# Kernel optimization log

Measured on AMD Instinct MI355X. Metric: run time of the kernel, lower is better.

Reference implementation:

```python
import jax, jax.numpy as jnp
import numpy as np
from jax import lax

B, HIST, FC, N, F = 64, 24, 24, 1000, 8
EMB, HID, NEMB, OUT = 32, 64, 1000, 1
IN = EMB + OUT  # GRU input dim


def setup_inputs() -> dict:
    key = jax.random.key(0)
    ks = jax.random.split(key, 11)
    X = jax.random.normal(ks[0], (B, HIST + FC, N, F), jnp.float32)
    idx = jax.random.randint(ks[1], (B, HIST + FC, N), 0, NEMB)
    X = X.at[..., -1].set(idx.astype(jnp.float32))  # last channel = spatial ids
    hn = jax.random.normal(ks[2], (B * N, HID), jnp.float32)
    xn = jax.random.normal(ks[3], (B, N, OUT), jnp.float32)
    s = 0.1
    emb_table = jax.random.normal(ks[4], (NEMB, EMB), jnp.float32) * s
    W_ih = jax.random.normal(ks[5], (3 * HID, IN), jnp.float32) * s
    W_hh = jax.random.normal(ks[6], (3 * HID, HID), jnp.float32) * s
    b_ih = jax.random.normal(ks[7], (3 * HID,), jnp.float32) * s
    b_hh = jax.random.normal(ks[8], (3 * HID,), jnp.float32) * s
    W_out = jax.random.normal(ks[9], (OUT, HID), jnp.float32) * s
    b_out = jax.random.normal(ks[10], (OUT,), jnp.float32) * s
    return {"X": X, "hn": hn, "xn": xn, "emb_table": emb_table,
            "W_ih": W_ih, "W_hh": W_hh, "b_ih": b_ih, "b_hh": b_hh,
            "W_out": W_out, "b_out": b_out}


def reference(X, hn, xn, emb_table, W_ih, W_hh, b_ih, b_hh, W_out, b_out):
    # indices for the forecast steps: [FC, B, N]
    idx_seq = X[:, :FC, :, -1].astype(jnp.int32).transpose(1, 0, 2)

    def step(carry, idx_t):
        h, x_prev = carry                      # h: [B*N, HID], x_prev: [B, N, 1]
        emb = emb_table[idx_t]                 # [B, N, EMB] gather
        x = jnp.concatenate([x_prev, emb], axis=-1).reshape(B * N, IN)
        gi = x @ W_ih.T + b_ih                 # [B*N, 3*HID]
        gh = h @ W_hh.T + b_hh
        i_r, i_z, i_n = jnp.split(gi, 3, axis=-1)
        h_r, h_z, h_n = jnp.split(gh, 3, axis=-1)
        r = jax.nn.sigmoid(i_r + h_r)
        z = jax.nn.sigmoid(i_z + h_z)
        n = jnp.tanh(i_n + r * h_n)
        h_new = (1.0 - z) * n + z * h
        out = h_new.reshape(B, N, HID) @ W_out.T + b_out  # [B, N, 1]
        return (h_new, out), out

    _, preds = lax.scan(step, (hn, xn), idx_seq)  # preds: [FC, B, N, 1]
    return preds.transpose(1, 0, 2, 3)            # [B, FC, N, 1]
```

## Files before the change

### kernel.cpp

```cpp
#include <hip/hip_runtime.h>
#include <math.h>

#define BB   64
#define FC   24
#define NN   1000
#define HID  64
#define EMBD 32
#define TT   48
#define FF   8
#define NEMB 1000
#define G3   192
#define INSZ 33

#define CPB  32
#define TPB  256
#define MT   2
#define AST  72

#define EPB  8

typedef __attribute__((ext_vector_type(8))) short bf16x8;
typedef __attribute__((ext_vector_type(4))) float f32x4;

static __device__ __forceinline__ unsigned short f2bf(float f) {
    unsigned u = __builtin_bit_cast(unsigned, f);
    u += 0x7FFFu + ((u >> 16) & 1u);
    return (unsigned short)(u >> 16);
}
static __device__ __forceinline__ float fast_sigmoid(float v) {
    float e = __builtin_amdgcn_exp2f(-1.4426950408889634f * v);
    return __builtin_amdgcn_rcpf(1.0f + e);
}
static __device__ __forceinline__ float fast_tanh(float v) {
    float vv = fminf(fmaxf(v, -15.0f), 15.0f);
    float e = __builtin_amdgcn_exp2f(2.8853900817779268f * vv);
    return 1.0f - 2.0f * __builtin_amdgcn_rcpf(e + 1.0f);
}

__global__ __launch_bounds__(256) void premul_kernel(
    const float* __restrict__ emb, const float* __restrict__ Wih,
    const float* __restrict__ bih, const float* __restrict__ bhh,
    float* __restrict__ P3)
{
    __shared__ float Wihs[INSZ * G3];
    __shared__ float xes[EPB * EMBD];
    const int tid = threadIdx.x;
    const int e0  = blockIdx.x * EPB;

    for (int i = tid; i < G3 * INSZ; i += 256) {
        int j = i / INSZ, k = i - j * INSZ;
        Wihs[k * G3 + j] = Wih[i];
    }
    xes[tid] = emb[(size_t)e0 * EMBD + tid];
    __syncthreads();

    const int el = tid >> 5;
    const float* xe = xes + el * EMBD;
    #pragma unroll
    for (int i = 0; i < G3 / 32; ++i) {
        int j = (tid & 31) + 32 * i;
        float acc = bih[j] + (j < 2 * HID ? bhh[j] : 0.0f);
        #pragma unroll
        for (int k = 0; k < EMBD; ++k)
            acc = fmaf(Wihs[(k + 1) * G3 + j], xe[k], acc);
        P3[(size_t)(e0 + el) * G3 + (j & 63) * 3 + (j >> 6)] = acc;
    }
}

__global__ __launch_bounds__(TPB) __attribute__((amdgpu_waves_per_eu(4)))
void gru_decoder(
    const float* __restrict__ X,
    const float* __restrict__ hn0,
    const float* __restrict__ xn,
    const float* __restrict__ Whh,
    const float* __restrict__ bhh,
    const float* __restrict__ Wih,
    const float* __restrict__ Wout,
    const float* __restrict__ bout,
    const float* __restrict__ P3,
    float* __restrict__ out)
{
    __shared__ __align__(16) unsigned short Abuf[CPB * AST];
    __shared__ int   idxbuf[FC * CPB];
    __shared__ float xbuf[CPB];

    const int tid  = threadIdx.x;
    const int lane = tid & 63;
    const int g    = tid >> 6;
    const int quad = lane >> 4;
    const int l15  = lane & 15;
    const int jcol = g * 16 + l15;
    const int rowb = quad * 4;
    const int cell0 = blockIdx.x * CPB;

    for (int e = tid; e < FC * CPB; e += TPB) {
        int t = e >> 5, m = e & 31;
        int cell = cell0 + m;
        int b = cell / NN, n = cell - b * NN;
        idxbuf[t * CPB + m] = (int)X[(((size_t)b * TT + t) * NN + n) * FF + 7];
    }
    if (tid < CPB) xbuf[tid] = xn[cell0 + tid];

    bf16x8 Bf[3][2];
    #pragma unroll
    for (int gate = 0; gate < 3; ++gate) {
        #pragma unroll
        for (int ks = 0; ks < 2; ++ks) {
            const float* src = Whh + (size_t)(gate * HID + jcol) * HID + ks * 32 + quad * 8;
            float4 lo = *(const float4*)src;
            float4 hi = *(const float4*)(src + 4);
            bf16x8 f;
            f[0] = (short)f2bf(lo.x); f[1] = (short)f2bf(lo.y);
            f[2] = (short)f2bf(lo.z); f[3] = (short)f2bf(lo.w);
            f[4] = (short)f2bf(hi.x); f[5] = (short)f2bf(hi.y);
            f[6] = (short)f2bf(hi.z); f[7] = (short)f2bf(hi.w);
            Bf[gate][ks] = f;
        }
    }

    const float w0r = Wih[(size_t)jcol * INSZ];
    const float w0z = Wih[(size_t)(HID + jcol) * INSZ];
    const float w0n = Wih[(size_t)(2 * HID + jcol) * INSZ];
    const float bhn = bhh[2 * HID + jcol];
    const float bout0 = bout[0];

    const int cd_m   = g * 8 + (lane & 7);
    const int kslice = lane >> 3;
    float wout_r[8];
    #pragma unroll
    for (int e2 = 0; e2 < 8; ++e2) wout_r[e2] = Wout[kslice * 8 + e2];
    const int cd_cell = cell0 + cd_m;
    const int cd_b = cd_cell / NN, cd_n = cd_cell - cd_b * NN;
    const size_t obase = (size_t)cd_b * FC * NN + cd_n;

    float hold[MT][4];
    #pragma unroll
    for (int mt = 0; mt < MT; ++mt) {
        #pragma unroll
        for (int rr = 0; rr < 4; ++rr) {
            int m = mt * 16 + rowb + rr;
            float h = hn0[((size_t)cell0 + m) * HID + jcol];
            hold[mt][rr] = h;
            Abuf[m * AST + jcol] = f2bf(h);
        }
    }
    __syncthreads();

    for (int t = 0; t < FC; ++t) {
        f32x4 accr[MT], accz[MT], accn[MT];
        #pragma unroll
        for (int mt = 0; mt < MT; ++mt) {
            const bf16x8 a0 = *(const bf16x8*)&Abuf[(mt * 16 + l15) * AST + quad * 8];
            const bf16x8 a1 = *(const bf16x8*)&Abuf[(mt * 16 + l15) * AST + 32 + quad * 8];
            f32x4 z4 = {0.f, 0.f, 0.f, 0.f};
            accr[mt] = __builtin_amdgcn_mfma_f32_16x16x32_bf16(a0, Bf[0][0], z4, 0, 0, 0);
            accr[mt] = __builtin_amdgcn_mfma_f32_16x16x32_bf16(a1, Bf[0][1], accr[mt], 0, 0, 0);
            accz[mt] = __builtin_amdgcn_mfma_f32_16x16x32_bf16(a0, Bf[1][0], z4, 0, 0, 0);
            accz[mt] = __builtin_amdgcn_mfma_f32_16x16x32_bf16(a1, Bf[1][1], accz[mt], 0, 0, 0);
            accn[mt] = __builtin_amdgcn_mfma_f32_16x16x32_bf16(a0, Bf[2][0], z4, 0, 0, 0);
            accn[mt] = __builtin_amdgcn_mfma_f32_16x16x32_bf16(a1, Bf[2][1], accn[mt], 0, 0, 0);
        }

        if (t > 0) {
            bf16x8 hv = *(const bf16x8*)&Abuf[cd_m * AST + kslice * 8];
            const unsigned* hv32 = (const unsigned*)&hv;
            float o = 0.f;
            #pragma unroll
            for (int q = 0; q < 4; ++q) {
                unsigned v = hv32[q];
                o = fmaf(wout_r[2 * q],     __builtin_bit_cast(float, v << 16),         o);
                o = fmaf(wout_r[2 * q + 1], __builtin_bit_cast(float, v & 0xFFFF0000u), o);
            }
            o += __shfl_xor(o, 8);
            o += __shfl_xor(o, 16);
            o += __shfl_xor(o, 32);
            if (lane < 8) {
                float oo = o + bout0;
                out[obase + (size_t)(t - 1) * NN] = oo;
                xbuf[cd_m] = oo;
            }
        }
        __syncthreads();

        #pragma unroll
        for (int mt = 0; mt < MT; ++mt) {
            #pragma unroll
            for (int rr = 0; rr < 4; ++rr) {
                int m   = mt * 16 + rowb + rr;
                int idx = idxbuf[t * CPB + m];
                float xp = xbuf[m];
                const float* pp = P3 + (size_t)idx * G3 + jcol * 3;
                float ar = fmaf(w0r, xp, pp[0]);
                float az = fmaf(w0z, xp, pp[1]);
                float an = fmaf(w0n, xp, pp[2]);
                float r  = fast_sigmoid(ar + accr[mt][rr]);
                float z  = fast_sigmoid(az + accz[mt][rr]);
                float nv = fast_tanh(an + r * (accn[mt][rr] + bhn));
                float hnew = nv + z * (hold[mt][rr] - nv);
                hold[mt][rr] = hnew;
                Abuf[m * AST + jcol] = f2bf(hnew);
            }
        }
        __syncthreads();
    }

    {
        bf16x8 hv = *(const bf16x8*)&Abuf[cd_m * AST + kslice * 8];
        const unsigned* hv32 = (const unsigned*)&hv;
        float o = 0.f;
        #pragma unroll
        for (int q = 0; q < 4; ++q) {
            unsigned v = hv32[q];
            o = fmaf(wout_r[2 * q],     __builtin_bit_cast(float, v << 16),         o);
            o = fmaf(wout_r[2 * q + 1], __builtin_bit_cast(float, v & 0xFFFF0000u), o);
        }
        o += __shfl_xor(o, 8);
        o += __shfl_xor(o, 16);
        o += __shfl_xor(o, 32);
        if (lane < 8) out[obase + (size_t)(FC - 1) * NN] = o + bout0;
    }
}

extern "C" void kernel_launch(void* const* d_in, const int* in_sizes, int n_in,
                              void* d_out, int out_size, void* d_ws, size_t ws_size,
                              hipStream_t stream) {
    (void)in_sizes; (void)n_in; (void)out_size; (void)ws_size;
    const float* X    = (const float*)d_in[0];
    const float* hn   = (const float*)d_in[1];
    const float* xn   = (const float*)d_in[2];
    const float* emb  = (const float*)d_in[3];
    const float* Wih  = (const float*)d_in[4];
    const float* Whh  = (const float*)d_in[5];
    const float* bih  = (const float*)d_in[6];
    const float* bhh  = (const float*)d_in[7];
    const float* Wout = (const float*)d_in[8];
    const float* bout = (const float*)d_in[9];
    float* out = (float*)d_out;
    float* P3  = (float*)d_ws;

    premul_kernel<<<NEMB / EPB, 256, 0, stream>>>(emb, Wih, bih, bhh, P3);

    const int blocks = (BB * NN) / CPB;
    gru_decoder<<<blocks, TPB, 0, stream>>>(X, hn, xn, Whh, bhh, Wih,
                                            Wout, bout, P3, out);
}
```

Baseline: 267.6 us.

## Fuse embedding input projection into GRU MFMA loop with split-bf16 precision

Drops the separate premul kernel that precomputed embedding-times-W_ih tables. Each step now stages the next step's embedding rows into shared memory as hi/lo bf16 pairs and computes the input projection with extra MFMAs, using a three-term split to keep near-fp32 accuracy. This removes one kernel launch and the per-step scattered P3 gathers, at the cost of more than doubling the MFMA count per step and adding embedding loads to the serial loop. It also changes the output-reduction lane mapping so each cell is reduced within 8 adjacent lanes.

```diff
diff --git a/kernel.cpp b/kernel.cpp
--- a/kernel.cpp
+++ b/kernel.cpp
@@ -8,18 +8,15 @@
 #define EMBD 32
 #define TT   48
 #define FF   8
-#define NEMB 1000
-#define G3   192
 #define INSZ 33
 
 #define CPB  32
 #define TPB  256
 #define MT   2
-#define AST  72
-
-#define EPB  8
+#define AST  136
 
 typedef __attribute__((ext_vector_type(8))) short bf16x8;
+typedef __attribute__((ext_vector_type(4))) short bf16x4;
 typedef __attribute__((ext_vector_type(4))) float f32x4;
 
 static __device__ __forceinline__ unsigned short f2bf(float f) {
@@ -27,6 +24,9 @@
     u += 0x7FFFu + ((u >> 16) & 1u);
     return (unsigned short)(u >> 16);
 }
+static __device__ __forceinline__ float bf2f(unsigned short h) {
+    return __builtin_bit_cast(float, (unsigned)h << 16);
+}
 static __device__ __forceinline__ float fast_sigmoid(float v) {
     float e = __builtin_amdgcn_exp2f(-1.4426950408889634f * v);
     return __builtin_amdgcn_rcpf(1.0f + e);
@@ -35,36 +35,6 @@
     float vv = fminf(fmaxf(v, -15.0f), 15.0f);
     float e = __builtin_amdgcn_exp2f(2.8853900817779268f * vv);
     return 1.0f - 2.0f * __builtin_amdgcn_rcpf(e + 1.0f);
-}
-
-__global__ __launch_bounds__(256) void premul_kernel(
-    const float* __restrict__ emb, const float* __restrict__ Wih,
-    const float* __restrict__ bih, const float* __restrict__ bhh,
-    float* __restrict__ P3)
-{
-    __shared__ float Wihs[INSZ * G3];
-    __shared__ float xes[EPB * EMBD];
-    const int tid = threadIdx.x;
-    const int e0  = blockIdx.x * EPB;
-
-    for (int i = tid; i < G3 * INSZ; i += 256) {
-        int j = i / INSZ, k = i - j * INSZ;
-        Wihs[k * G3 + j] = Wih[i];
-    }
-    xes[tid] = emb[(size_t)e0 * EMBD + tid];
-    __syncthreads();
-
-    const int el = tid >> 5;
-    const float* xe = xes + el * EMBD;
-    #pragma unroll
-    for (int i = 0; i < G3 / 32; ++i) {
-        int j = (tid & 31) + 32 * i;
-        float acc = bih[j] + (j < 2 * HID ? bhh[j] : 0.0f);
-        #pragma unroll
-        for (int k = 0; k < EMBD; ++k)
-            acc = fmaf(Wihs[(k + 1) * G3 + j], xe[k], acc);
-        P3[(size_t)(e0 + el) * G3 + (j & 63) * 3 + (j >> 6)] = acc;
-    }
 }
 
 __global__ __launch_bounds__(TPB) __attribute__((amdgpu_waves_per_eu(4)))
@@ -72,12 +42,13 @@
     const float* __restrict__ X,
     const float* __restrict__ hn0,
     const float* __restrict__ xn,
+    const float* __restrict__ emb,
+    const float* __restrict__ Wih,
     const float* __restrict__ Whh,
+    const float* __restrict__ bih,
     const float* __restrict__ bhh,
-    const float* __restrict__ Wih,
     const float* __restrict__ Wout,
     const float* __restrict__ bout,
-    const float* __restrict__ P3,
     float* __restrict__ out)
 {
     __shared__ __align__(16) unsigned short Abuf[CPB * AST];
@@ -100,6 +71,7 @@
         idxbuf[t * CPB + m] = (int)X[(((size_t)b * TT + t) * NN + n) * FF + 7];
     }
     if (tid < CPB) xbuf[tid] = xn[cell0 + tid];
+    __syncthreads();
 
     bf16x8 Bf[3][2];
     #pragma unroll
@@ -117,15 +89,33 @@
             Bf[gate][ks] = f;
         }
     }
+    bf16x8 Bf2h[3], Bf2l[3];
+    #pragma unroll
+    for (int gate = 0; gate < 3; ++gate) {
+        const float* src = Wih + (size_t)(gate * HID + jcol) * INSZ + 1 + quad * 8;
+        bf16x8 fh, fl;
+        #pragma unroll
+        for (int e2 = 0; e2 < 8; ++e2) {
+            float w = src[e2];
+            unsigned short h = f2bf(w);
+            fh[e2] = (short)h;
+            fl[e2] = (short)f2bf(w - bf2f(h));
+        }
+        Bf2h[gate] = fh;
+        Bf2l[gate] = fl;
+    }
 
     const float w0r = Wih[(size_t)jcol * INSZ];
     const float w0z = Wih[(size_t)(HID + jcol) * INSZ];
     const float w0n = Wih[(size_t)(2 * HID + jcol) * INSZ];
+    const float br  = bih[jcol] + bhh[jcol];
+    const float bz  = bih[HID + jcol] + bhh[HID + jcol];
+    const float bn  = bih[2 * HID + jcol];
     const float bhn = bhh[2 * HID + jcol];
     const float bout0 = bout[0];
 
-    const int cd_m   = g * 8 + (lane & 7);
-    const int kslice = lane >> 3;
+    const int kslice = lane & 7;
+    const int cd_m   = g * 8 + (lane >> 3);
     float wout_r[8];
     #pragma unroll
     for (int e2 = 0; e2 < 8; ++e2) wout_r[e2] = Wout[kslice * 8 + e2];
@@ -144,21 +134,48 @@
             Abuf[m * AST + jcol] = f2bf(h);
         }
     }
+    {
+        const int c = tid >> 3, kg = tid & 7;
+        int idx = idxbuf[c];
+        float4 v = *(const float4*)(emb + (size_t)idx * EMBD + kg * 4);
+        bf16x4 wh, wl;
+        float vv[4] = {v.x, v.y, v.z, v.w};
+        #pragma unroll
+        for (int q = 0; q < 4; ++q) {
+            unsigned short h = f2bf(vv[q]);
+            wh[q] = (short)h;
+            wl[q] = (short)f2bf(vv[q] - bf2f(h));
+        }
+        *(bf16x4*)&Abuf[c * AST + HID + kg * 4]      = wh;
+        *(bf16x4*)&Abuf[c * AST + HID + 32 + kg * 4] = wl;
+    }
     __syncthreads();
 
     for (int t = 0; t < FC; ++t) {
-        f32x4 accr[MT], accz[MT], accn[MT];
+        f32x4 accr[MT], accz[MT], acch[MT], acce[MT];
         #pragma unroll
         for (int mt = 0; mt < MT; ++mt) {
-            const bf16x8 a0 = *(const bf16x8*)&Abuf[(mt * 16 + l15) * AST + quad * 8];
-            const bf16x8 a1 = *(const bf16x8*)&Abuf[(mt * 16 + l15) * AST + 32 + quad * 8];
+            const int rb = (mt * 16 + l15) * AST;
+            const bf16x8 a0  = *(const bf16x8*)&Abuf[rb + quad * 8];
+            const bf16x8 a1  = *(const bf16x8*)&Abuf[rb + 32 + quad * 8];
+            const bf16x8 a2h = *(const bf16x8*)&Abuf[rb + HID + quad * 8];
+            const bf16x8 a2l = *(const bf16x8*)&Abuf[rb + HID + 32 + quad * 8];
             f32x4 z4 = {0.f, 0.f, 0.f, 0.f};
-            accr[mt] = __builtin_amdgcn_mfma_f32_16x16x32_bf16(a0, Bf[0][0], z4, 0, 0, 0);
-            accr[mt] = __builtin_amdgcn_mfma_f32_16x16x32_bf16(a1, Bf[0][1], accr[mt], 0, 0, 0);
-            accz[mt] = __builtin_amdgcn_mfma_f32_16x16x32_bf16(a0, Bf[1][0], z4, 0, 0, 0);
-            accz[mt] = __builtin_amdgcn_mfma_f32_16x16x32_bf16(a1, Bf[1][1], accz[mt], 0, 0, 0);
-            accn[mt] = __builtin_amdgcn_mfma_f32_16x16x32_bf16(a0, Bf[2][0], z4, 0, 0, 0);
-            accn[mt] = __builtin_amdgcn_mfma_f32_16x16x32_bf16(a1, Bf[2][1], accn[mt], 0, 0, 0);
+            accr[mt] = __builtin_amdgcn_mfma_f32_16x16x32_bf16(a0,  Bf[0][0], z4, 0, 0, 0);
+            accr[mt] = __builtin_amdgcn_mfma_f32_16x16x32_bf16(a1,  Bf[0][1], accr[mt], 0, 0, 0);
+            accr[mt] = __builtin_amdgcn_mfma_f32_16x16x32_bf16(a2h, Bf2h[0],  accr[mt], 0, 0, 0);
+            accr[mt] = __builtin_amdgcn_mfma_f32_16x16x32_bf16(a2l, Bf2h[0],  accr[mt], 0, 0, 0);
+            accr[mt] = __builtin_amdgcn_mfma_f32_16x16x32_bf16(a2h, Bf2l[0],  accr[mt], 0, 0, 0);
+            accz[mt] = __builtin_amdgcn_mfma_f32_16x16x32_bf16(a0,  Bf[1][0], z4, 0, 0, 0);
+            accz[mt] = __builtin_amdgcn_mfma_f32_16x16x32_bf16(a1,  Bf[1][1], accz[mt], 0, 0, 0);
+            accz[mt] = __builtin_amdgcn_mfma_f32_16x16x32_bf16(a2h, Bf2h[1],  accz[mt], 0, 0, 0);
+            accz[mt] = __builtin_amdgcn_mfma_f32_16x16x32_bf16(a2l, Bf2h[1],  accz[mt], 0, 0, 0);
+            accz[mt] = __builtin_amdgcn_mfma_f32_16x16x32_bf16(a2h, Bf2l[1],  accz[mt], 0, 0, 0);
+            acch[mt] = __builtin_amdgcn_mfma_f32_16x16x32_bf16(a0,  Bf[2][0], z4, 0, 0, 0);
+            acch[mt] = __builtin_amdgcn_mfma_f32_16x16x32_bf16(a1,  Bf[2][1], acch[mt], 0, 0, 0);
+            acce[mt] = __builtin_amdgcn_mfma_f32_16x16x32_bf16(a2h, Bf2h[2],  z4, 0, 0, 0);
+            acce[mt] = __builtin_amdgcn_mfma_f32_16x16x32_bf16(a2l, Bf2h[2],  acce[mt], 0, 0, 0);
+            acce[mt] = __builtin_amdgcn_mfma_f32_16x16x32_bf16(a2h, Bf2l[2],  acce[mt], 0, 0, 0);
         }
 
         if (t > 0) {
@@ -171,10 +188,10 @@
                 o = fmaf(wout_r[2 * q],     __builtin_bit_cast(float, v << 16),         o);
                 o = fmaf(wout_r[2 * q + 1], __builtin_bit_cast(float, v & 0xFFFF0000u), o);
             }
-            o += __shfl_xor(o, 8);
-            o += __shfl_xor(o, 16);
-            o += __shfl_xor(o, 32);
-            if (lane < 8) {
+            o += __shfl_xor(o, 1);
+            o += __shfl_xor(o, 2);
+            o += __shfl_xor(o, 4);
+            if ((lane & 7) == 0) {
                 float oo = o + bout0;
                 out[obase + (size_t)(t - 1) * NN] = oo;
                 xbuf[cd_m] = oo;
@@ -187,19 +204,32 @@
             #pragma unroll
             for (int rr = 0; rr < 4; ++rr) {
                 int m   = mt * 16 + rowb + rr;
-                int idx = idxbuf[t * CPB + m];
                 float xp = xbuf[m];
-                const float* pp = P3 + (size_t)idx * G3 + jcol * 3;
-                float ar = fmaf(w0r, xp, pp[0]);
-                float az = fmaf(w0z, xp, pp[1]);
-                float an = fmaf(w0n, xp, pp[2]);
+                float ar = fmaf(w0r, xp, br);
+                float az = fmaf(w0z, xp, bz);
+                float an = fmaf(w0n, xp, bn) + acce[mt][rr];
                 float r  = fast_sigmoid(ar + accr[mt][rr]);
                 float z  = fast_sigmoid(az + accz[mt][rr]);
-                float nv = fast_tanh(an + r * (accn[mt][rr] + bhn));
+                float nv = fast_tanh(an + r * (acch[mt][rr] + bhn));
                 float hnew = nv + z * (hold[mt][rr] - nv);
                 hold[mt][rr] = hnew;
                 Abuf[m * AST + jcol] = f2bf(hnew);
             }
+        }
+        if (t + 1 < FC) {
+            const int c = tid >> 3, kg = tid & 7;
+            int idx = idxbuf[(t + 1) * CPB + c];
+            float4 v = *(const float4*)(emb + (size_t)idx * EMBD + kg * 4);
+            bf16x4 wh, wl;
+            float vv[4] = {v.x, v.y, v.z, v.w};
+            #pragma unroll
+            for (int q = 0; q < 4; ++q) {
+                unsigned short h = f2bf(vv[q]);
+                wh[q] = (short)h;
+                wl[q] = (short)f2bf(vv[q] - bf2f(h));
+            }
+            *(bf16x4*)&Abuf[c * AST + HID + kg * 4]      = wh;
+            *(bf16x4*)&Abuf[c * AST + HID + 32 + kg * 4] = wl;
         }
         __syncthreads();
     }
@@ -214,17 +244,17 @@
             o = fmaf(wout_r[2 * q],     __builtin_bit_cast(float, v << 16),         o);
             o = fmaf(wout_r[2 * q + 1], __builtin_bit_cast(float, v & 0xFFFF0000u), o);
         }
-        o += __shfl_xor(o, 8);
-        o += __shfl_xor(o, 16);
-        o += __shfl_xor(o, 32);
-        if (lane < 8) out[obase + (size_t)(FC - 1) * NN] = o + bout0;
+        o += __shfl_xor(o, 1);
+        o += __shfl_xor(o, 2);
+        o += __shfl_xor(o, 4);
+        if ((lane & 7) == 0) out[obase + (size_t)(FC - 1) * NN] = o + bout0;
     }
 }
 
 extern "C" void kernel_launch(void* const* d_in, const int* in_sizes, int n_in,
                               void* d_out, int out_size, void* d_ws, size_t ws_size,
                               hipStream_t stream) {
-    (void)in_sizes; (void)n_in; (void)out_size; (void)ws_size;
+    (void)in_sizes; (void)n_in; (void)out_size; (void)d_ws; (void)ws_size;
     const float* X    = (const float*)d_in[0];
     const float* hn   = (const float*)d_in[1];
     const float* xn   = (const float*)d_in[2];
@@ -236,11 +266,8 @@
     const float* Wout = (const float*)d_in[8];
     const float* bout = (const float*)d_in[9];
     float* out = (float*)d_out;
-    float* P3  = (float*)d_ws;
-
-    premul_kernel<<<NEMB / EPB, 256, 0, stream>>>(emb, Wih, bih, bhh, P3);
 
     const int blocks = (BB * NN) / CPB;
-    gru_decoder<<<blocks, TPB, 0, stream>>>(X, hn, xn, Whh, bhh, Wih,
-                                            Wout, bout, P3, out);
-}
+    gru_decoder<<<blocks, TPB, 0, stream>>>(X, hn, xn, emb, Wih, Whh,
+                                            bih, bhh, Wout, bout, out);
+}
```

Result: slower. 430.2 us (+60.7%).
